# Kernel optimization log

Hardware: AMD Instinct MI355X
Metric: run time of the kernel (lower is better)

## Reference

```python
import jax, jax.numpy as jnp
from jax import lax
import numpy as np

L, B, D_IN, D_OUT, D_MLP = 64, 32, 512, 512, 128
WINDOWS = [1, 3]
FEATS = [256, 128]
C = sum(FEATS)  # 384
EPS = 1e-5


def _leaky(x):
    return jnp.where(x >= 0, x, 0.1 * x)


def setup_inputs() -> dict:
    key = jax.random.key(0)
    ks = jax.random.split(key, 16)
    s = lambda k, shp: (jax.random.normal(k, shp, jnp.float32) * 0.02)
    inp = {}
    inp["x"] = jax.random.normal(ks[0], (L, B, D_IN), jnp.float32)
    inp["xs_mask"] = jnp.ones((L, B), jnp.float32)
    # conv + batchnorm params per window
    inp["conv_w0"] = s(ks[1], (FEATS[0], 1, D_IN * WINDOWS[0]))
    inp["conv_b0"] = jnp.zeros((FEATS[0],), jnp.float32)
    inp["gamma0"] = jnp.ones((FEATS[0],), jnp.float32)
    inp["beta0"] = jnp.zeros((FEATS[0],), jnp.float32)
    inp["conv_w1"] = s(ks[2], (FEATS[1], 1, D_IN * WINDOWS[1]))
    inp["conv_b1"] = jnp.zeros((FEATS[1],), jnp.float32)
    inp["gamma1"] = jnp.ones((FEATS[1],), jnp.float32)
    inp["beta1"] = jnp.zeros((FEATS[1],), jnp.float32)
    inp["w0"] = s(ks[3], (2 * C, D_MLP)); inp["b0"] = jnp.zeros((D_MLP,), jnp.float32)
    inp["w1"] = s(ks[4], (D_MLP, D_MLP)); inp["b1"] = jnp.zeros((D_MLP,), jnp.float32)
    inp["w2"] = s(ks[5], (D_MLP, D_MLP)); inp["b2"] = jnp.zeros((D_MLP,), jnp.float32)
    inp["w3"] = s(ks[6], (D_MLP, D_MLP)); inp["b3"] = jnp.zeros((D_MLP,), jnp.float32)
    # output MLP: Linear(d_mlp->d_mlp), Linear(d_mlp->d_out)
    inp["w4"] = s(ks[7], (D_MLP, D_MLP)); inp["b4"] = jnp.zeros((D_MLP,), jnp.float32)
    inp["w5"] = s(ks[8], (D_MLP, D_OUT)); inp["b5"] = jnp.zeros((D_OUT,), jnp.float32)
    return inp


def reference(x, xs_mask, conv_w0, conv_b0, gamma0, beta0, conv_w1, conv_b1,
              gamma1, beta1, w0, b0, w1, b1, w2, b2, w3, b3, w4, b4, w5, b5):
    # x: (L, B, E)
    x = x * xs_mask[:, :, None]
    xf = jnp.transpose(x, (1, 0, 2)).reshape(B, 1, L * D_IN)  # (B, 1, L*E)

    # CNN front-end: Conv1d(stride=d_in) + BatchNorm1d (batch stats) + LeakyReLU
    feats = []
    for win, cw, cb, g, bt in [(WINDOWS[0], conv_w0, conv_b0, gamma0, beta0),
                               (WINDOWS[1], conv_w1, conv_b1, gamma1, beta1)]:
        pad = (win - 1) // 2 * D_IN
        y = lax.conv_general_dilated(xf, cw, window_strides=(D_IN,),
                                     padding=[(pad, pad)],
                                     dimension_numbers=("NCH", "OIH", "NCH"))
        y = y + cb[None, :, None]  # (B, C_k, L)
        m = y.mean(axis=(0, 2))
        v = y.var(axis=(0, 2))  # biased var, as torch BN training mode
        y = (y - m[None, :, None]) / jnp.sqrt(v[None, :, None] + EPS)
        y = y * g[None, :, None] + bt[None, :, None]
        feats.append(_leaky(y))
    h = jnp.concatenate(feats, axis=1)          # (B, C, L)
    h = jnp.transpose(h, (2, 0, 1))             # (L, B, C)
    h = h * xs_mask[:, :, None]

    # Graph propagation: pairwise concat + first linear, split over concat halves
    # cat([h_i, h_j]) @ w0 == h_i @ w0[:C] + h_j @ w0[C:]  (avoids (L,L,B,2C) tensor)
    a = jnp.einsum("lbc,cd->lbd", h, w0[:C])    # (L, B, d_mlp)
    bb = jnp.einsum("lbc,cd->lbd", h, w0[C:])   # (L, B, d_mlp)
    p = _leaky(a[:, None, :, :] + bb[None, :, :, :] + b0)  # (L, L, B, d_mlp)
    p = _leaky(p @ w1 + b1)
    p = _leaky(p @ w2 + b2)
    p = _leaky(p @ w3 + b3)
    p = p * xs_mask[:, None, :, None]
    p = p.mean(axis=1)                          # (L, B, d_mlp)

    out = _leaky(p @ w4 + b4)
    out = _leaky(out @ w5 + b5)                 # (L, B, d_out)
    return out * xs_mask[:, :, None]
```

## Files before the change

### kernel.cpp

```cpp
#include <hip/hip_runtime.h>


#define BB 32
#define CCH 384

__device__ __forceinline__ float leaky(float x) { return fmaxf(x, 0.1f * x); }

typedef _Float16 f16x8 __attribute__((ext_vector_type(8)));
typedef float f32x4 __attribute__((ext_vector_type(4)));

union F8 { uint4 q; f16x8 h; };
union H2 { _Float16 f[2]; uint32_t u; };

__device__ __forceinline__ void split2(float d0, float d1,
                                       uint32_t& hw, uint32_t& lw) {
  H2 h, l;
  h.f[0] = (_Float16)d0; h.f[1] = (_Float16)d1;
  l.f[0] = (_Float16)((d0 - (float)h.f[0]) * 2048.0f);
  l.f[1] = (_Float16)((d1 - (float)h.f[1]) * 2048.0f);
  hw = h.u; lw = l.u;
}

__global__ __launch_bounds__(256) void conv_kernel(
    const float* __restrict__ x, const float* __restrict__ mask,
    const float* __restrict__ cw0, const float* __restrict__ cw1,
    float* __restrict__ yG)
{
  __shared__ float As[32 * 36];
  __shared__ float Ws[32 * 132];
  int bx = blockIdx.x;
  int rt = bx & 63;
  int ct = bx >> 6;
  int row0 = rt * 32;
  int tid = threadIdx.x;

  const float* wbase; int wstride;
  if (ct < 2) { wbase = cw0 + ct * 128 * 512; wstride = 512; }
  else        { wbase = cw1 + (ct - 2) * 512; wstride = 1536; }

  int sr  = tid >> 3;
  int sk4 = (tid & 7) * 4;
  const float* xrow = x + (row0 + sr) * 512;
  float mval = mask[row0 + sr];

  int r4 = (tid >> 5) * 4;
  int c4 = (tid & 31) * 4;

  float acc[4][4] = {{0.f,0.f,0.f,0.f},{0.f,0.f,0.f,0.f},
                     {0.f,0.f,0.f,0.f},{0.f,0.f,0.f,0.f}};
#pragma unroll 1
  for (int k0 = 0; k0 < 512; k0 += 32) {
    float4 xv = *(const float4*)(xrow + k0 + sk4);
    float4 wv[4];
#pragma unroll
    for (int rep = 0; rep < 4; ++rep) {
      int slot = rep * 256 + tid;
      int c = slot >> 3;
      int kq4 = (slot & 7) * 4;
      wv[rep] = *(const float4*)(wbase + c * wstride + k0 + kq4);
    }
    __syncthreads();
    As[(sk4 + 0) * 36 + sr] = xv.x * mval;
    As[(sk4 + 1) * 36 + sr] = xv.y * mval;
    As[(sk4 + 2) * 36 + sr] = xv.z * mval;
    As[(sk4 + 3) * 36 + sr] = xv.w * mval;
#pragma unroll
    for (int rep = 0; rep < 4; ++rep) {
      int slot = rep * 256 + tid;
      int c = slot >> 3;
      int kq4 = (slot & 7) * 4;
      Ws[(kq4 + 0) * 132 + c] = wv[rep].x;
      Ws[(kq4 + 1) * 132 + c] = wv[rep].y;
      Ws[(kq4 + 2) * 132 + c] = wv[rep].z;
      Ws[(kq4 + 3) * 132 + c] = wv[rep].w;
    }
    __syncthreads();
#pragma unroll
    for (int kk = 0; kk < 32; ++kk) {
      float4 a = *(const float4*)&As[kk * 36 + r4];
      float4 w = *(const float4*)&Ws[kk * 132 + c4];
      float av[4] = {a.x, a.y, a.z, a.w};
      float wv2[4] = {w.x, w.y, w.z, w.w};
#pragma unroll
      for (int ri = 0; ri < 4; ++ri)
#pragma unroll
        for (int ci = 0; ci < 4; ++ci)
          acc[ri][ci] = fmaf(av[ri], wv2[ci], acc[ri][ci]);
    }
  }
#pragma unroll
  for (int ci = 0; ci < 4; ++ci)
    *(float4*)&yG[(ct * 128 + c4 + ci) * 2048 + row0 + r4] =
        make_float4(acc[0][ci], acc[1][ci], acc[2][ci], acc[3][ci]);
}

__global__ __launch_bounds__(256) void stats_kernel(
    const float* __restrict__ yG,
    const float* __restrict__ g0, const float* __restrict__ be0,
    const float* __restrict__ g1, const float* __restrict__ be1,
    float* __restrict__ scale, float* __restrict__ shift)
{
  int c = blockIdx.x;
  int tid = threadIdx.x;
  float s = 0.f, s2 = 0.f;
  if (c < 256) {
    const float* src = yG + c * 2048 + tid * 8;
    float4 v0 = *(const float4*)(src);
    float4 v1 = *(const float4*)(src + 4);
    s  = v0.x + v0.y + v0.z + v0.w + v1.x + v1.y + v1.z + v1.w;
    s2 = v0.x*v0.x + v0.y*v0.y + v0.z*v0.z + v0.w*v0.w
       + v1.x*v1.x + v1.y*v1.y + v1.z*v1.z + v1.w*v1.w;
  } else {
    int cc = c - 256;
    const float* p0 = yG + (256 + cc) * 2048;
    const float* p1 = yG + (384 + cc) * 2048;
    const float* p2 = yG + (512 + cc) * 2048;
#pragma unroll
    for (int j = 0; j < 8; ++j) {
      int e = tid * 8 + j;
      float v = p1[e];
      if (e >= 32)   v += p0[e - 32];
      if (e < 2016)  v += p2[e + 32];
      s += v; s2 += v * v;
    }
  }
#pragma unroll
  for (int off = 32; off > 0; off >>= 1) {
    s  += __shfl_down(s, off);
    s2 += __shfl_down(s2, off);
  }
  __shared__ float rs[4], rs2[4];
  int wid = tid >> 6;
  if ((tid & 63) == 0) { rs[wid] = s; rs2[wid] = s2; }
  __syncthreads();
  if (tid == 0) {
    float S  = rs[0] + rs[1] + rs[2] + rs[3];
    float S2 = rs2[0] + rs2[1] + rs2[2] + rs2[3];
    float mean = S * (1.f / 2048.f);
    float var  = S2 * (1.f / 2048.f) - mean * mean;
    float g  = (c < 256) ? g0[c] : g1[c - 256];
    float be = (c < 256) ? be0[c] : be1[c - 256];
    float sc = g / sqrtf(var + 1e-5f);
    scale[c] = sc;
    shift[c] = be - mean * sc;
  }
}

__global__ __launch_bounds__(256) void ab_kernel(
    const float* __restrict__ yG, const float* __restrict__ scale,
    const float* __restrict__ shift, const float* __restrict__ mask,
    const float* __restrict__ w0,
    const float* __restrict__ w1, const float* __restrict__ w2,
    const float* __restrict__ w3, uint32_t* __restrict__ wpk,
    float* __restrict__ a_arr, float* __restrict__ bb_arr)
{
  int bx = blockIdx.x;
  int tid = threadIdx.x;
  if (bx >= 256) {
    int e = (bx - 256) * 256 + tid;
    int L = e >> 13;
    int r = e & 8191;
    int k2 = r >> 7, n = r & 127;
    int k = k2 * 2;
    const float* w = (L == 0) ? w1 : (L == 1) ? w2 : w3;
    uint32_t hw, lw;
    split2(w[k * 128 + n], w[(k + 1) * 128 + n], hw, lw);
    wpk[L * 8192 + n * 64 + k2] = hw;
    wpk[24576 + L * 8192 + n * 64 + k2] = lw;
    return;
  }
  __shared__ float As[32 * 36];
  __shared__ float Ws[32 * 68];
  int rt = bx & 63, ct = bx >> 6;
  int row0 = rt * 32, n0 = ct * 64;
  int r4 = (tid >> 5) * 4;
  int n2 = (tid & 31) * 2;
  int scc = tid >> 3, srr4 = (tid & 7) * 4;
  int wnn8 = (tid & 7) * 8;
  const float* wbase = (n0 < 128) ? (w0 + n0) : (w0 + CCH * 128 + (n0 - 128));
  float4 mv = *(const float4*)(mask + row0 + srr4);

  float acc[4][2] = {{0.f, 0.f}};
#pragma unroll 1
  for (int c0 = 0; c0 < 384; c0 += 32) {
    int c = c0 + scc;
    float4 yv;
    if (c < 256) {
      yv = *(const float4*)(yG + c * 2048 + row0 + srr4);
    } else {
      int cc = c - 256;
      yv = *(const float4*)(yG + (384 + cc) * 2048 + row0 + srr4);
      if (rt > 0) {
        float4 u = *(const float4*)(yG + (256 + cc) * 2048 + row0 + srr4 - 32);
        yv.x += u.x; yv.y += u.y; yv.z += u.z; yv.w += u.w;
      }
      if (rt < 63) {
        float4 u = *(const float4*)(yG + (512 + cc) * 2048 + row0 + srr4 + 32);
        yv.x += u.x; yv.y += u.y; yv.z += u.z; yv.w += u.w;
      }
    }
    float sc = scale[c], sh = shift[c];
    float4 wv0 = *(const float4*)(wbase + c * 128 + wnn8);
    float4 wv1 = *(const float4*)(wbase + c * 128 + wnn8 + 4);
    __syncthreads();
    float4 hv;
    hv.x = leaky(fmaf(yv.x, sc, sh)) * mv.x;
    hv.y = leaky(fmaf(yv.y, sc, sh)) * mv.y;
    hv.z = leaky(fmaf(yv.z, sc, sh)) * mv.z;
    hv.w = leaky(fmaf(yv.w, sc, sh)) * mv.w;
    *(float4*)&As[scc * 36 + srr4] = hv;
    *(float4*)&Ws[scc * 68 + wnn8] = wv0;
    *(float4*)&Ws[scc * 68 + wnn8 + 4] = wv1;
    __syncthreads();
#pragma unroll
    for (int cc = 0; cc < 32; ++cc) {
      float4 a = *(const float4*)&As[cc * 36 + r4];
      float2 w = *(const float2*)&Ws[cc * 68 + n2];
      acc[0][0] = fmaf(a.x, w.x, acc[0][0]); acc[0][1] = fmaf(a.x, w.y, acc[0][1]);
      acc[1][0] = fmaf(a.y, w.x, acc[1][0]); acc[1][1] = fmaf(a.y, w.y, acc[1][1]);
      acc[2][0] = fmaf(a.z, w.x, acc[2][0]); acc[2][1] = fmaf(a.z, w.y, acc[2][1]);
      acc[3][0] = fmaf(a.w, w.x, acc[3][0]); acc[3][1] = fmaf(a.w, w.y, acc[3][1]);
    }
  }
  float* dst; int nd;
  if (n0 < 128) { dst = a_arr; nd = n0; } else { dst = bb_arr; nd = n0 - 128; }
#pragma unroll
  for (int ri = 0; ri < 4; ++ri)
    *(float2*)&dst[(row0 + r4 + ri) * 128 + nd + n2] = make_float2(acc[ri][0], acc[ri][1]);
}

__global__ __launch_bounds__(512) void pair_kernel(
    const float* __restrict__ a_arr, const float* __restrict__ bb_arr,
    const float* __restrict__ b0, const uint32_t* __restrict__ wpk,
    const float* __restrict__ b1, const float* __restrict__ b2,
    const float* __restrict__ b3,
    const float* __restrict__ w4, const float* __restrict__ b4,
    const float* __restrict__ w5, const float* __restrict__ b5,
    const float* __restrict__ mask, float* __restrict__ out)
{
  __shared__ uint32_t Ahs[128 * 68];
  __shared__ uint32_t Als[128 * 68];
  int i = blockIdx.x, bp = blockIdx.y;
  int tid = threadIdx.x;

#pragma unroll 1
  for (int it = 0; it < 4; ++it) {
    int idx = it * 512 + tid;
    int r   = idx >> 4;
    int k8  = (idx & 15) * 8;
    int db  = r >> 6, j = r & 63;
    int bq  = bp * 2 + db;
    const float* ap = a_arr + (i * BB + bq) * 128 + k8;
    const float* bbp = bb_arr + (j * BB + bq) * 128 + k8;
    const float* zp = b0 + k8;
    float d[8];
#pragma unroll
    for (int t = 0; t < 8; t += 4) {
      float4 av = *(const float4*)(ap + t);
      float4 bv = *(const float4*)(bbp + t);
      float4 zv = *(const float4*)(zp + t);
      d[t+0] = leaky(av.x + bv.x + zv.x);
      d[t+1] = leaky(av.y + bv.y + zv.y);
      d[t+2] = leaky(av.z + bv.z + zv.z);
      d[t+3] = leaky(av.w + bv.w + zv.w);
    }
    uint4 hq, lq;
    split2(d[0], d[1], hq.x, lq.x);
    split2(d[2], d[3], hq.y, lq.y);
    split2(d[4], d[5], hq.z, lq.z);
    split2(d[6], d[7], hq.w, lq.w);
    *(uint4*)&Ahs[r * 68 + k8 / 2] = hq;
    *(uint4*)&Als[r * 68 + k8 / 2] = lq;
  }
  __syncthreads();

  int wid = __builtin_amdgcn_readfirstlane(tid >> 6);
  int wm = wid & 1, wn = wid >> 1;
  int lane = tid & 63;
  int m16 = lane & 15, q = lane >> 4;

  f32x4 hi[4][2], cr[4][2];

#pragma unroll 1
  for (int L = 0; L < 3; ++L) {
    const uint32_t* WhL = wpk + L * 8192;
    const uint32_t* WlL = wpk + 24576 + L * 8192;
    const float* Bv = (L == 0) ? b1 : (L == 1) ? b2 : b3;
#pragma unroll
    for (int mt = 0; mt < 4; ++mt)
#pragma unroll
      for (int nt = 0; nt < 2; ++nt) {
        hi[mt][nt] = (f32x4){0.f, 0.f, 0.f, 0.f};
        cr[mt][nt] = (f32x4){0.f, 0.f, 0.f, 0.f};
      }

    F8 Wh[2], Wl[2], Whn[2], Wln[2];
#pragma unroll
    for (int nt = 0; nt < 2; ++nt) {
      int wrow = wn * 32 + nt * 16 + m16;
      Wh[nt].q = *(const uint4*)(WhL + wrow * 64 + q * 4);
      Wl[nt].q = *(const uint4*)(WlL + wrow * 64 + q * 4);
    }

#pragma unroll
    for (int ks = 0; ks < 4; ++ks) {
      int koff2 = ks * 16 + q * 4;
      if (ks < 3) {
#pragma unroll
        for (int nt = 0; nt < 2; ++nt) {
          int wrow = wn * 32 + nt * 16 + m16;
          Whn[nt].q = *(const uint4*)(WhL + wrow * 64 + koff2 + 16);
          Wln[nt].q = *(const uint4*)(WlL + wrow * 64 + koff2 + 16);
        }
      }
#pragma unroll
      for (int mt = 0; mt < 4; ++mt) {
        int arow = wm * 64 + mt * 16 + m16;
        F8 Ah, Al;
        Ah.q = *(const uint4*)&Ahs[arow * 68 + koff2];
        Al.q = *(const uint4*)&Als[arow * 68 + koff2];
#pragma unroll
        for (int nt = 0; nt < 2; ++nt) {
          hi[mt][nt] = __builtin_amdgcn_mfma_f32_16x16x32_f16(
              Ah.h, Wh[nt].h, hi[mt][nt], 0, 0, 0);
          cr[mt][nt] = __builtin_amdgcn_mfma_f32_16x16x32_f16(
              Ah.h, Wl[nt].h, cr[mt][nt], 0, 0, 0);
          cr[mt][nt] = __builtin_amdgcn_mfma_f32_16x16x32_f16(
              Al.h, Wh[nt].h, cr[mt][nt], 0, 0, 0);
        }
      }
#pragma unroll
      for (int nt = 0; nt < 2; ++nt) { Wh[nt] = Whn[nt]; Wl[nt] = Wln[nt]; }
    }

    float bias[2];
#pragma unroll
    for (int nt = 0; nt < 2; ++nt) bias[nt] = Bv[wn * 32 + nt * 16 + m16];

    if (L < 2) {
      __syncthreads();
      int par = lane & 1;
#pragma unroll
      for (int mt = 0; mt < 4; ++mt)
#pragma unroll
        for (int nt = 0; nt < 2; ++nt) {
          int colw = (wn * 32 + nt * 16 + (m16 & ~1)) >> 1;
#pragma unroll
          for (int rg = 0; rg < 4; ++rg) {
            float d = leaky(hi[mt][nt][rg] + cr[mt][nt][rg] * (1.0f / 2048.0f)
                            + bias[nt]);
            float dn = __shfl_xor(d, 1, 64);
            float de = par ? dn : d;
            float do_ = par ? d : dn;
            uint32_t hw, lw;
            split2(de, do_, hw, lw);
            int row = wm * 64 + mt * 16 + q * 4 + rg;
            if (par) Als[row * 68 + colw] = lw;
            else     Ahs[row * 68 + colw] = hw;
          }
        }
      __syncthreads();
    } else {
      float s[2] = {0.f, 0.f};
#pragma unroll
      for (int nt = 0; nt < 2; ++nt)
#pragma unroll
        for (int mt = 0; mt < 4; ++mt)
#pragma unroll
          for (int rg = 0; rg < 4; ++rg)
            s[nt] += leaky(hi[mt][nt][rg] + cr[mt][nt][rg] * (1.0f / 2048.0f)
                           + bias[nt]);
      int browp = i * BB + bp * 2 + wm;
      float mfac = (1.0f / 64.0f) * mask[browp];
#pragma unroll
      for (int nt = 0; nt < 2; ++nt) {
        s[nt] += __shfl_xor(s[nt], 16, 64);
        s[nt] += __shfl_xor(s[nt], 32, 64);
      }
      __syncthreads();
      float* scratch = (float*)Ahs;
      float* Pm = scratch;
      float* Tp = scratch + 256;
      float* T4 = scratch + 768;
      if (lane < 16) {
#pragma unroll
        for (int nt = 0; nt < 2; ++nt)
          Pm[wm * 128 + wn * 32 + nt * 16 + m16] = s[nt] * mfac;
      }
      __syncthreads();
      {
        int row = tid >> 8;
        int ch  = (tid >> 7) & 1;
        int k   = tid & 127;
        const float* pm  = Pm + row * 128 + ch * 64;
        const float* w4c = w4 + ch * 64 * 128 + k;
        float t = ch ? 0.f : b4[k];
#pragma unroll 4
        for (int c0 = 0; c0 < 64; c0 += 4) {
          float4 pv = *(const float4*)&pm[c0];
          t = fmaf(pv.x, w4c[(c0 + 0) * 128], t);
          t = fmaf(pv.y, w4c[(c0 + 1) * 128], t);
          t = fmaf(pv.z, w4c[(c0 + 2) * 128], t);
          t = fmaf(pv.w, w4c[(c0 + 3) * 128], t);
        }
        Tp[(row * 2 + ch) * 128 + k] = t;
      }
      __syncthreads();
      if (tid < 256) {
        int row = tid >> 7, k = tid & 127;
        T4[row * 128 + k] = leaky(Tp[row * 256 + k] + Tp[row * 256 + 128 + k]);
      }
      __syncthreads();
      {
        int kk = tid;
        float o0 = b5[kk], o1 = o0;
#pragma unroll 4
        for (int c0 = 0; c0 < 128; c0 += 4) {
          float4 ta = *(const float4*)&T4[c0];
          float4 tb = *(const float4*)&T4[128 + c0];
          float w0v = w5[(c0 + 0) * 512 + kk];
          float w1v = w5[(c0 + 1) * 512 + kk];
          float w2v = w5[(c0 + 2) * 512 + kk];
          float w3v = w5[(c0 + 3) * 512 + kk];
          o0 = fmaf(ta.x, w0v, o0); o1 = fmaf(tb.x, w0v, o1);
          o0 = fmaf(ta.y, w1v, o0); o1 = fmaf(tb.y, w1v, o1);
          o0 = fmaf(ta.z, w2v, o0); o1 = fmaf(tb.z, w2v, o1);
          o0 = fmaf(ta.w, w3v, o0); o1 = fmaf(tb.w, w3v, o1);
        }
        int brow0 = i * BB + bp * 2;
        float m0 = mask[brow0], m1 = mask[brow0 + 1];
        out[brow0 * 512 + kk]       = leaky(o0) * m0;
        out[(brow0 + 1) * 512 + kk] = leaky(o1) * m1;
      }
    }
  }
}

extern "C" void kernel_launch(void* const* d_in, const int* in_sizes, int n_in,
                              void* d_out, int out_size, void* d_ws, size_t ws_size,
                              hipStream_t stream) {
  const float* x    = (const float*)d_in[0];
  const float* mask = (const float*)d_in[1];
  const float* cw0  = (const float*)d_in[2];
  const float* g0   = (const float*)d_in[4];
  const float* be0  = (const float*)d_in[5];
  const float* cw1  = (const float*)d_in[6];
  const float* g1   = (const float*)d_in[8];
  const float* be1  = (const float*)d_in[9];
  const float* w0   = (const float*)d_in[10];
  const float* b0   = (const float*)d_in[11];
  const float* w1   = (const float*)d_in[12];
  const float* b1   = (const float*)d_in[13];
  const float* w2   = (const float*)d_in[14];
  const float* b2   = (const float*)d_in[15];
  const float* w3   = (const float*)d_in[16];
  const float* b3   = (const float*)d_in[17];
  const float* w4   = (const float*)d_in[18];
  const float* b4   = (const float*)d_in[19];
  const float* w5   = (const float*)d_in[20];
  const float* b5   = (const float*)d_in[21];

  float* ws     = (float*)d_ws;
  float* yG     = ws;
  uint32_t* wpk = (uint32_t*)(ws + 1310720);
  float* scale  = ws + 1359872;
  float* shift  = ws + 1360256;
  float* a_arr  = ws + 1360640;
  float* bb_arr = ws + 1622784;
  float* outp   = (float*)d_out;

  conv_kernel<<<320, 256, 0, stream>>>(x, mask, cw0, cw1, yG);
  stats_kernel<<<384, 256, 0, stream>>>(yG, g0, be0, g1, be1, scale, shift);
  ab_kernel<<<352, 256, 0, stream>>>(yG, scale, shift, mask, w0,
                                     w1, w2, w3, wpk, a_arr, bb_arr);
  dim3 g5(64, 16);
  pair_kernel<<<g5, 512, 0, stream>>>(a_arr, bb_arr, b0, wpk, b1, b2, b3,
                                      w4, b4, w5, b5, mask, outp);
}
```

Before: 259.8 us.

## Move conv to split-fp16 MFMA, fuse BN stats via atomics, drop stats kernel

The conv front-end becomes a split-fp16 (hi/lo) MFMA GEMM. The window-3 taps are folded into the K dimension with shifted row loads, so the kernel writes the final summed channels directly. Per-channel sum and sum-of-squares are accumulated with atomics in the conv epilogue, and the separate stats kernel is removed. The ab kernel now computes scale and shift itself and no longer reconstructs window-3 sums from three partial tap outputs. This cuts one launch and redundant yG traffic, at the cost of a memset, atomic contention, and the 3-product fp16 emulation's accuracy.

```diff
diff --git a/kernel.cpp b/kernel.cpp
--- a/kernel.cpp
+++ b/kernel.cpp
@@ -24,132 +24,160 @@
 __global__ __launch_bounds__(256) void conv_kernel(
     const float* __restrict__ x, const float* __restrict__ mask,
     const float* __restrict__ cw0, const float* __restrict__ cw1,
-    float* __restrict__ yG)
+    float* __restrict__ yG, float* __restrict__ Ssum, float* __restrict__ Ssq)
 {
-  __shared__ float As[32 * 36];
-  __shared__ float Ws[32 * 132];
+  __shared__ uint32_t Ah[64 * 68], Al[64 * 68];
+  __shared__ uint32_t Bh[64 * 68], Bl[64 * 68];
   int bx = blockIdx.x;
-  int rt = bx & 63;
-  int ct = bx >> 6;
-  int row0 = rt * 32;
+  int nb = bx % 6, mb = bx / 6;
+  int n0 = nb * 64;
+  int row0 = mb * 64;
+  bool w3 = (nb >= 4);
+  int nch = w3 ? 12 : 4;
+  const float* wbase = w3 ? (cw1 + (n0 - 256) * 1536) : (cw0 + n0 * 512);
+  int wK = w3 ? 1536 : 512;
+
   int tid = threadIdx.x;
-
-  const float* wbase; int wstride;
-  if (ct < 2) { wbase = cw0 + ct * 128 * 512; wstride = 512; }
-  else        { wbase = cw1 + (ct - 2) * 512; wstride = 1536; }
-
-  int sr  = tid >> 3;
-  int sk4 = (tid & 7) * 4;
-  const float* xrow = x + (row0 + sr) * 512;
-  float mval = mask[row0 + sr];
-
-  int r4 = (tid >> 5) * 4;
-  int c4 = (tid & 31) * 4;
-
-  float acc[4][4] = {{0.f,0.f,0.f,0.f},{0.f,0.f,0.f,0.f},
-                     {0.f,0.f,0.f,0.f},{0.f,0.f,0.f,0.f}};
+  int wid = __builtin_amdgcn_readfirstlane(tid >> 6);
+  int wm = wid & 1, wn2 = wid >> 1;
+  int lane = tid & 63;
+  int m16 = lane & 15, q = lane >> 4;
+
+  f32x4 hi[2][2], cr[2][2];
+#pragma unroll
+  for (int a = 0; a < 2; ++a)
+#pragma unroll
+    for (int b = 0; b < 2; ++b) {
+      hi[a][b] = (f32x4){0.f, 0.f, 0.f, 0.f};
+      cr[a][b] = (f32x4){0.f, 0.f, 0.f, 0.f};
+    }
+
 #pragma unroll 1
-  for (int k0 = 0; k0 < 512; k0 += 32) {
-    float4 xv = *(const float4*)(xrow + k0 + sk4);
-    float4 wv[4];
-#pragma unroll
-    for (int rep = 0; rep < 4; ++rep) {
-      int slot = rep * 256 + tid;
-      int c = slot >> 3;
-      int kq4 = (slot & 7) * 4;
-      wv[rep] = *(const float4*)(wbase + c * wstride + k0 + kq4);
-    }
+  for (int ch = 0; ch < nch; ++ch) {
+    int kg0 = ch * 128;
+    int tap = kg0 >> 9;
+    int d0 = kg0 & 511;
+    int shift = w3 ? (tap - 1) * 32 : 0;
     __syncthreads();
-    As[(sk4 + 0) * 36 + sr] = xv.x * mval;
-    As[(sk4 + 1) * 36 + sr] = xv.y * mval;
-    As[(sk4 + 2) * 36 + sr] = xv.z * mval;
-    As[(sk4 + 3) * 36 + sr] = xv.w * mval;
-#pragma unroll
-    for (int rep = 0; rep < 4; ++rep) {
-      int slot = rep * 256 + tid;
-      int c = slot >> 3;
-      int kq4 = (slot & 7) * 4;
-      Ws[(kq4 + 0) * 132 + c] = wv[rep].x;
-      Ws[(kq4 + 1) * 132 + c] = wv[rep].y;
-      Ws[(kq4 + 2) * 132 + c] = wv[rep].z;
-      Ws[(kq4 + 3) * 132 + c] = wv[rep].w;
+#pragma unroll 1
+    for (int it = 0; it < 4; ++it) {
+      int idx = it * 256 + tid;
+      int r = idx >> 4;
+      int k8 = (idx & 15) * 8;
+      float d[8];
+      int rowg = row0 + r + shift;
+      if ((unsigned)rowg < 2048u) {
+        float mv = mask[rowg];
+        const float* xp = x + rowg * 512 + d0 + k8;
+        float4 a0 = *(const float4*)xp;
+        float4 a1 = *(const float4*)(xp + 4);
+        d[0] = a0.x * mv; d[1] = a0.y * mv; d[2] = a0.z * mv; d[3] = a0.w * mv;
+        d[4] = a1.x * mv; d[5] = a1.y * mv; d[6] = a1.z * mv; d[7] = a1.w * mv;
+      } else {
+#pragma unroll
+        for (int t2 = 0; t2 < 8; ++t2) d[t2] = 0.f;
+      }
+      uint4 hq, lq;
+      split2(d[0], d[1], hq.x, lq.x);
+      split2(d[2], d[3], hq.y, lq.y);
+      split2(d[4], d[5], hq.z, lq.z);
+      split2(d[6], d[7], hq.w, lq.w);
+      *(uint4*)&Ah[r * 68 + k8 / 2] = hq;
+      *(uint4*)&Al[r * 68 + k8 / 2] = lq;
+      const float* wp = wbase + r * wK + kg0 + k8;
+      float4 b0v = *(const float4*)wp;
+      float4 b1v = *(const float4*)(wp + 4);
+      split2(b0v.x, b0v.y, hq.x, lq.x);
+      split2(b0v.z, b0v.w, hq.y, lq.y);
+      split2(b1v.x, b1v.y, hq.z, lq.z);
+      split2(b1v.z, b1v.w, hq.w, lq.w);
+      *(uint4*)&Bh[r * 68 + k8 / 2] = hq;
+      *(uint4*)&Bl[r * 68 + k8 / 2] = lq;
     }
     __syncthreads();
 #pragma unroll
-    for (int kk = 0; kk < 32; ++kk) {
-      float4 a = *(const float4*)&As[kk * 36 + r4];
-      float4 w = *(const float4*)&Ws[kk * 132 + c4];
-      float av[4] = {a.x, a.y, a.z, a.w};
-      float wv2[4] = {w.x, w.y, w.z, w.w};
-#pragma unroll
-      for (int ri = 0; ri < 4; ++ri)
-#pragma unroll
-        for (int ci = 0; ci < 4; ++ci)
-          acc[ri][ci] = fmaf(av[ri], wv2[ci], acc[ri][ci]);
-    }
-  }
-#pragma unroll
-  for (int ci = 0; ci < 4; ++ci)
-    *(float4*)&yG[(ct * 128 + c4 + ci) * 2048 + row0 + r4] =
-        make_float4(acc[0][ci], acc[1][ci], acc[2][ci], acc[3][ci]);
+    for (int ks = 0; ks < 4; ++ks) {
+      int koff = ks * 16 + q * 4;
+      F8 bh[2], bl[2];
+#pragma unroll
+      for (int nt = 0; nt < 2; ++nt) {
+        int br = wn2 * 32 + nt * 16 + m16;
+        bh[nt].q = *(const uint4*)&Bh[br * 68 + koff];
+        bl[nt].q = *(const uint4*)&Bl[br * 68 + koff];
+      }
+#pragma unroll
+      for (int mt = 0; mt < 2; ++mt) {
+        int ar = wm * 32 + mt * 16 + m16;
+        F8 ah, al;
+        ah.q = *(const uint4*)&Ah[ar * 68 + koff];
+        al.q = *(const uint4*)&Al[ar * 68 + koff];
+#pragma unroll
+        for (int nt = 0; nt < 2; ++nt) {
+          hi[mt][nt] = __builtin_amdgcn_mfma_f32_16x16x32_f16(
+              ah.h, bh[nt].h, hi[mt][nt], 0, 0, 0);
+          cr[mt][nt] = __builtin_amdgcn_mfma_f32_16x16x32_f16(
+              ah.h, bl[nt].h, cr[mt][nt], 0, 0, 0);
+          cr[mt][nt] = __builtin_amdgcn_mfma_f32_16x16x32_f16(
+              al.h, bh[nt].h, cr[mt][nt], 0, 0, 0);
+        }
+      }
+    }
+  }
+
+  float y[2][2][4];
+#pragma unroll
+  for (int mt = 0; mt < 2; ++mt)
+#pragma unroll
+    for (int nt = 0; nt < 2; ++nt)
+#pragma unroll
+      for (int rg = 0; rg < 4; ++rg)
+        y[mt][nt][rg] = hi[mt][nt][rg] + cr[mt][nt][rg] * (1.0f / 2048.0f);
+
+#pragma unroll
+  for (int nt = 0; nt < 2; ++nt) {
+    float s = 0.f, s2 = 0.f;
+#pragma unroll
+    for (int mt = 0; mt < 2; ++mt)
+#pragma unroll
+      for (int rg = 0; rg < 4; ++rg) {
+        float v = y[mt][nt][rg];
+        s += v; s2 += v * v;
+      }
+    s  += __shfl_xor(s, 16, 64);  s  += __shfl_xor(s, 32, 64);
+    s2 += __shfl_xor(s2, 16, 64); s2 += __shfl_xor(s2, 32, 64);
+    if (lane < 16) {
+      int c = n0 + wn2 * 32 + nt * 16 + m16;
+      atomicAdd(&Ssum[c], s);
+      atomicAdd(&Ssq[c], s2);
+    }
+  }
+
+  __syncthreads();
+  float* Yl = (float*)Ah;
+#pragma unroll
+  for (int mt = 0; mt < 2; ++mt)
+#pragma unroll
+    for (int nt = 0; nt < 2; ++nt)
+#pragma unroll
+      for (int rg = 0; rg < 4; ++rg)
+        Yl[(wn2 * 32 + nt * 16 + m16) * 68 + wm * 32 + mt * 16 + q * 4 + rg] =
+            y[mt][nt][rg];
+  __syncthreads();
+  {
+    int c = tid >> 2, seg = (tid & 3) * 16;
+#pragma unroll
+    for (int j = 0; j < 16; j += 4)
+      *(float4*)&yG[(n0 + c) * 2048 + row0 + seg + j] =
+          *(const float4*)&Yl[c * 68 + seg + j];
+  }
 }
 
-__global__ __launch_bounds__(256) void stats_kernel(
-    const float* __restrict__ yG,
+__global__ __launch_bounds__(256) void ab_kernel(
+    const float* __restrict__ yG, const float* __restrict__ Ssum,
+    const float* __restrict__ Ssq,
     const float* __restrict__ g0, const float* __restrict__ be0,
     const float* __restrict__ g1, const float* __restrict__ be1,
-    float* __restrict__ scale, float* __restrict__ shift)
-{
-  int c = blockIdx.x;
-  int tid = threadIdx.x;
-  float s = 0.f, s2 = 0.f;
-  if (c < 256) {
-    const float* src = yG + c * 2048 + tid * 8;
-    float4 v0 = *(const float4*)(src);
-    float4 v1 = *(const float4*)(src + 4);
-    s  = v0.x + v0.y + v0.z + v0.w + v1.x + v1.y + v1.z + v1.w;
-    s2 = v0.x*v0.x + v0.y*v0.y + v0.z*v0.z + v0.w*v0.w
-       + v1.x*v1.x + v1.y*v1.y + v1.z*v1.z + v1.w*v1.w;
-  } else {
-    int cc = c - 256;
-    const float* p0 = yG + (256 + cc) * 2048;
-    const float* p1 = yG + (384 + cc) * 2048;
-    const float* p2 = yG + (512 + cc) * 2048;
-#pragma unroll
-    for (int j = 0; j < 8; ++j) {
-      int e = tid * 8 + j;
-      float v = p1[e];
-      if (e >= 32)   v += p0[e - 32];
-      if (e < 2016)  v += p2[e + 32];
-      s += v; s2 += v * v;
-    }
-  }
-#pragma unroll
-  for (int off = 32; off > 0; off >>= 1) {
-    s  += __shfl_down(s, off);
-    s2 += __shfl_down(s2, off);
-  }
-  __shared__ float rs[4], rs2[4];
-  int wid = tid >> 6;
-  if ((tid & 63) == 0) { rs[wid] = s; rs2[wid] = s2; }
-  __syncthreads();
-  if (tid == 0) {
-    float S  = rs[0] + rs[1] + rs[2] + rs[3];
-    float S2 = rs2[0] + rs2[1] + rs2[2] + rs2[3];
-    float mean = S * (1.f / 2048.f);
-    float var  = S2 * (1.f / 2048.f) - mean * mean;
-    float g  = (c < 256) ? g0[c] : g1[c - 256];
-    float be = (c < 256) ? be0[c] : be1[c - 256];
-    float sc = g / sqrtf(var + 1e-5f);
-    scale[c] = sc;
-    shift[c] = be - mean * sc;
-  }
-}
-
-__global__ __launch_bounds__(256) void ab_kernel(
-    const float* __restrict__ yG, const float* __restrict__ scale,
-    const float* __restrict__ shift, const float* __restrict__ mask,
-    const float* __restrict__ w0,
+    const float* __restrict__ mask, const float* __restrict__ w0,
     const float* __restrict__ w1, const float* __restrict__ w2,
     const float* __restrict__ w3, uint32_t* __restrict__ wpk,
     float* __restrict__ a_arr, float* __restrict__ bb_arr)
@@ -171,6 +199,19 @@
   }
   __shared__ float As[32 * 36];
   __shared__ float Ws[32 * 68];
+  __shared__ float scs[384], shs[384];
+  for (int c = tid; c < 384; c += 256) {
+    float Sv = Ssum[c], S2v = Ssq[c];
+    float mean = Sv * (1.f / 2048.f);
+    float var  = S2v * (1.f / 2048.f) - mean * mean;
+    float g  = (c < 256) ? g0[c] : g1[c - 256];
+    float be = (c < 256) ? be0[c] : be1[c - 256];
+    float sc = g / sqrtf(var + 1e-5f);
+    scs[c] = sc;
+    shs[c] = be - mean * sc;
+  }
+  __syncthreads();
+
   int rt = bx & 63, ct = bx >> 6;
   int row0 = rt * 32, n0 = ct * 64;
   int r4 = (tid >> 5) * 4;
@@ -184,22 +225,8 @@
 #pragma unroll 1
   for (int c0 = 0; c0 < 384; c0 += 32) {
     int c = c0 + scc;
-    float4 yv;
-    if (c < 256) {
-      yv = *(const float4*)(yG + c * 2048 + row0 + srr4);
-    } else {
-      int cc = c - 256;
-      yv = *(const float4*)(yG + (384 + cc) * 2048 + row0 + srr4);
-      if (rt > 0) {
-        float4 u = *(const float4*)(yG + (256 + cc) * 2048 + row0 + srr4 - 32);
-        yv.x += u.x; yv.y += u.y; yv.z += u.z; yv.w += u.w;
-      }
-      if (rt < 63) {
-        float4 u = *(const float4*)(yG + (512 + cc) * 2048 + row0 + srr4 + 32);
-        yv.x += u.x; yv.y += u.y; yv.z += u.z; yv.w += u.w;
-      }
-    }
-    float sc = scale[c], sh = shift[c];
+    float4 yv = *(const float4*)(yG + c * 2048 + row0 + srr4);
+    float sc = scs[c], sh = shs[c];
     float4 wv0 = *(const float4*)(wbase + c * 128 + wnn8);
     float4 wv1 = *(const float4*)(wbase + c * 128 + wnn8 + 4);
     __syncthreads();
@@ -390,11 +417,11 @@
       __syncthreads();
       {
         int row = tid >> 8;
-        int ch  = (tid >> 7) & 1;
+        int chh = (tid >> 7) & 1;
         int k   = tid & 127;
-        const float* pm  = Pm + row * 128 + ch * 64;
-        const float* w4c = w4 + ch * 64 * 128 + k;
-        float t = ch ? 0.f : b4[k];
+        const float* pm  = Pm + row * 128 + chh * 64;
+        const float* w4c = w4 + chh * 64 * 128 + k;
+        float t = chh ? 0.f : b4[k];
 #pragma unroll 4
         for (int c0 = 0; c0 < 64; c0 += 4) {
           float4 pv = *(const float4*)&pm[c0];
@@ -403,7 +430,7 @@
           t = fmaf(pv.z, w4c[(c0 + 2) * 128], t);
           t = fmaf(pv.w, w4c[(c0 + 3) * 128], t);
         }
-        Tp[(row * 2 + ch) * 128 + k] = t;
+        Tp[(row * 2 + chh) * 128 + k] = t;
       }
       __syncthreads();
       if (tid < 256) {
@@ -461,18 +488,18 @@
   const float* b5   = (const float*)d_in[21];
 
   float* ws     = (float*)d_ws;
-  float* yG     = ws;
-  uint32_t* wpk = (uint32_t*)(ws + 1310720);
-  float* scale  = ws + 1359872;
-  float* shift  = ws + 1360256;
-  float* a_arr  = ws + 1360640;
-  float* bb_arr = ws + 1622784;
+  float* Ssum   = ws;
+  float* Ssq    = ws + 384;
+  float* yG     = ws + 768;
+  uint32_t* wpk = (uint32_t*)(ws + 787200);
+  float* a_arr  = ws + 836352;
+  float* bb_arr = ws + 1098496;
   float* outp   = (float*)d_out;
 
-  conv_kernel<<<320, 256, 0, stream>>>(x, mask, cw0, cw1, yG);
-  stats_kernel<<<384, 256, 0, stream>>>(yG, g0, be0, g1, be1, scale, shift);
-  ab_kernel<<<352, 256, 0, stream>>>(yG, scale, shift, mask, w0,
-                                     w1, w2, w3, wpk, a_arr, bb_arr);
+  hipMemsetAsync(Ssum, 0, 768 * sizeof(float), stream);
+  conv_kernel<<<192, 256, 0, stream>>>(x, mask, cw0, cw1, yG, Ssum, Ssq);
+  ab_kernel<<<352, 256, 0, stream>>>(yG, Ssum, Ssq, g0, be0, g1, be1,
+                                     mask, w0, w1, w2, w3, wpk, a_arr, bb_arr);
   dim3 g5(64, 16);
   pair_kernel<<<g5, 512, 0, stream>>>(a_arr, bb_arr, b0, wpk, b1, b2, b3,
                                       w4, b4, w5, b5, mask, outp);
```

After: 257.8 us. No clear change (-0.8%).
